# Kernel tuning notes

Hardware: AMD Instinct MI355X
Metric: run time of the kernel (lower is better)

The kernel has to match this reference:

```python
import jax, jax.numpy as jnp
import numpy as np

N, E, IN, H1, H2 = 100000, 3200000, 128, 64, 64


def setup_inputs() -> dict:
    key = jax.random.key(0)
    ks = jax.random.split(key, 6)
    return {
        "edge_index": jax.random.randint(ks[0], (2, E), 0, N),
        "edge_weight": jax.random.uniform(ks[1], (E,), jnp.float32),
        "emb": jax.random.normal(ks[2], (N, IN), jnp.float32) * 0.05,  # xavier-initialized node embeddings
        "W1": jax.random.normal(ks[3], (IN, H1), jnp.float32) / np.sqrt(IN),
        "b1": jnp.zeros((H1,), jnp.float32),
        "W2": jax.random.normal(ks[4], (H1, H2), jnp.float32) / np.sqrt(H1),
        "b2": jnp.zeros((H2,), jnp.float32),
    }


def _digcn_conv(x, edge_index, edge_weight, W, b):
    # DIGCNConv: dense transform, then weighted sparse neighborhood sum-aggregation.
    x = x @ W                                              # [N, d_out]
    msg = edge_weight[:, None] * x[edge_index[0]]          # gather sources -> [E, d_out]
    out = jax.ops.segment_sum(msg, edge_index[1], num_segments=x.shape[0])  # scatter-add to targets
    return out + b


def reference(edge_index, edge_weight, emb, W1, b1, W2, b2):
    h = jax.nn.relu(_digcn_conv(emb, edge_index, edge_weight, W1, b1))
    # F.dropout with training=False is identity (inference mode)
    return _digcn_conv(h, edge_index, edge_weight, W2, b2)
```

## Files before the change

### kernel.cpp

```cpp
#include <hip/hip_runtime.h>
#include <hip/hip_bf16.h>

#define NNODES 100000
#define DIN 128
#define DH 64
#define SRCMASK 0x1FFFF
#define BSH2 8
#define BN2 256
#define NBUCK2 ((NNODES + BN2 - 1) >> BSH2)
#define NCAP 8960
#define EPB 8192
#define MAXBLK 512
#define OVFCAP 4096

typedef short s16x8 __attribute__((ext_vector_type(8)));
typedef float f32x4 __attribute__((ext_vector_type(4)));

static __device__ __forceinline__ short f2bf(float f) {
  __hip_bfloat16 h = __float2bfloat16(f);
  return *reinterpret_cast<short*>(&h);
}
static __device__ __forceinline__ float bf2f(short s) {
  return __uint_as_float(((unsigned)(unsigned short)s) << 16);
}


__global__ __launch_bounds__(256, 4) void gemm1_mfma(
    const float* __restrict__ emb, const float* __restrict__ W1,
    __hip_bfloat16* __restrict__ x1, int N) {
  __shared__ short Bhi[4 * 4 * 64 * 8];
  __shared__ short Blo[4 * 4 * 64 * 8];
  int tid = threadIdx.x;

  for (int idx = tid; idx < 8192; idx += 256) {
    int i = idx & 7, ln = (idx >> 3) & 63, ct = (idx >> 9) & 3, kc = idx >> 11;
    int k = kc * 32 + (ln >> 4) * 8 + i;
    int col = ct * 16 + (ln & 15);
    float w = W1[k * DH + col];
    short h = f2bf(w);
    Bhi[idx] = h;
    Blo[idx] = f2bf(w - bf2f(h));
  }
  __syncthreads();

  int lane = tid & 63, wv = tid >> 6;
  int r0 = (blockIdx.x * 8 + wv * 2) * 16;
  if (r0 >= N) return;

  const int rA = lane & 15, g = lane >> 4;
  f32x4 acc[2][4] = {};

#pragma unroll
  for (int kc = 0; kc < 4; ++kc) {
    s16x8 ahi[2], alo[2];
#pragma unroll
    for (int rt = 0; rt < 2; ++rt) {
      int r = r0 + rt * 16 + rA;
      float av[8];
      if (r < N) {
        const float4* ap = (const float4*)(emb + (long)r * DIN + kc * 32 + g * 8);
        float4 v0 = ap[0], v1 = ap[1];
        av[0] = v0.x; av[1] = v0.y; av[2] = v0.z; av[3] = v0.w;
        av[4] = v1.x; av[5] = v1.y; av[6] = v1.z; av[7] = v1.w;
      } else {
#pragma unroll
        for (int i = 0; i < 8; ++i) av[i] = 0.f;
      }
#pragma unroll
      for (int i = 0; i < 8; ++i) {
        short h = f2bf(av[i]);
        ahi[rt][i] = h;
        alo[rt][i] = f2bf(av[i] - bf2f(h));
      }
    }
#pragma unroll
    for (int ct = 0; ct < 4; ++ct) {
      int fo = ((kc * 4 + ct) * 64 + lane) * 8;
      s16x8 bh = *(const s16x8*)&Bhi[fo];
      s16x8 bl = *(const s16x8*)&Blo[fo];
#pragma unroll
      for (int rt = 0; rt < 2; ++rt) {
        acc[rt][ct] = __builtin_amdgcn_mfma_f32_16x16x32_bf16(ahi[rt], bh, acc[rt][ct], 0, 0, 0);
        acc[rt][ct] = __builtin_amdgcn_mfma_f32_16x16x32_bf16(alo[rt], bh, acc[rt][ct], 0, 0, 0);
        acc[rt][ct] = __builtin_amdgcn_mfma_f32_16x16x32_bf16(ahi[rt], bl, acc[rt][ct], 0, 0, 0);
      }
    }
  }

#pragma unroll
  for (int rt = 0; rt < 2; ++rt) {
#pragma unroll
    for (int j = 0; j < 4; ++j) {
      int row = r0 + rt * 16 + g * 4 + j;
      if (row < N) {
#pragma unroll
        for (int ct = 0; ct < 4; ++ct)
          x1[(long)row * DH + ct * 16 + rA] = __float2bfloat16(acc[rt][ct][j]);
      }
    }
  }
}

__global__ __launch_bounds__(256, 4) void gemm2_mfma(
    const float* __restrict__ agg, const float* __restrict__ W2,
    const float* __restrict__ b1, __hip_bfloat16* __restrict__ x2, int N) {
  __shared__ short Bhi[2 * 4 * 64 * 8];
  __shared__ short Blo[2 * 4 * 64 * 8];
  int tid = threadIdx.x;

  for (int idx = tid; idx < 4096; idx += 256) {
    int i = idx & 7, ln = (idx >> 3) & 63, ct = (idx >> 9) & 3, kc = (idx >> 11) & 1;
    int k = kc * 32 + (ln >> 4) * 8 + i;
    int col = ct * 16 + (ln & 15);
    float w = W2[k * DH + col];
    short h = f2bf(w);
    Bhi[idx] = h;
    Blo[idx] = f2bf(w - bf2f(h));
  }
  __syncthreads();

  int lane = tid & 63, wv = tid >> 6;
  int r0 = (blockIdx.x * 8 + wv * 2) * 16;
  if (r0 >= N) return;

  const int rA = lane & 15, g = lane >> 4;
  f32x4 acc[2][4] = {};

#pragma unroll
  for (int kc = 0; kc < 2; ++kc) {
    const float4* bp = (const float4*)(b1 + kc * 32 + g * 8);
    float4 b0 = bp[0], b4 = bp[1];
    float bv[8] = {b0.x, b0.y, b0.z, b0.w, b4.x, b4.y, b4.z, b4.w};
    s16x8 ahi[2], alo[2];
#pragma unroll
    for (int rt = 0; rt < 2; ++rt) {
      int r = r0 + rt * 16 + rA;
      float av[8];
      if (r < N) {
        const float4* ap = (const float4*)(agg + (long)r * DH + kc * 32 + g * 8);
        float4 v0 = ap[0], v1 = ap[1];
        av[0] = v0.x; av[1] = v0.y; av[2] = v0.z; av[3] = v0.w;
        av[4] = v1.x; av[5] = v1.y; av[6] = v1.z; av[7] = v1.w;
      } else {
#pragma unroll
        for (int i = 0; i < 8; ++i) av[i] = -1e30f;
      }
#pragma unroll
      for (int i = 0; i < 8; ++i) {
        float a = fmaxf(av[i] + bv[i], 0.f);
        short h = f2bf(a);
        ahi[rt][i] = h;
        alo[rt][i] = f2bf(a - bf2f(h));
      }
    }
#pragma unroll
    for (int ct = 0; ct < 4; ++ct) {
      int fo = ((kc * 4 + ct) * 64 + lane) * 8;
      s16x8 bh = *(const s16x8*)&Bhi[fo];
      s16x8 bl = *(const s16x8*)&Blo[fo];
#pragma unroll
      for (int rt = 0; rt < 2; ++rt) {
        acc[rt][ct] = __builtin_amdgcn_mfma_f32_16x16x32_bf16(ahi[rt], bh, acc[rt][ct], 0, 0, 0);
        acc[rt][ct] = __builtin_amdgcn_mfma_f32_16x16x32_bf16(alo[rt], bh, acc[rt][ct], 0, 0, 0);
        acc[rt][ct] = __builtin_amdgcn_mfma_f32_16x16x32_bf16(ahi[rt], bl, acc[rt][ct], 0, 0, 0);
      }
    }
  }

#pragma unroll
  for (int rt = 0; rt < 2; ++rt) {
#pragma unroll
    for (int j = 0; j < 4; ++j) {
      int row = r0 + rt * 16 + g * 4 + j;
      if (row < N) {
#pragma unroll
        for (int ct = 0; ct < 4; ++ct)
          x2[(long)row * DH + ct * 16 + rA] = __float2bfloat16(acc[rt][ct][j]);
      }
    }
  }
}


__global__ __launch_bounds__(512, 6) void block_sort(
    const int* __restrict__ srcs, const int* __restrict__ dsts,
    const float* __restrict__ w, int* __restrict__ spk,
    unsigned char* __restrict__ sdl, unsigned short* __restrict__ offTab, int E) {
  __shared__ int stageP[EPB];
  __shared__ unsigned char stageD[EPB];
  __shared__ int hist[512];
  __shared__ int sc[512];
  __shared__ int cur[512];
  int tid = threadIdx.x, blk = blockIdx.x;
  int e0 = blk * EPB;

  hist[tid] = 0;
  __syncthreads();

  int pk[16], bd[16];
#pragma unroll
  for (int i = 0; i < 16; ++i) {
    int e = e0 + i * 512 + tid;
    if (e < E) {
      int s = srcs[e], d = dsts[e];
      float wv = w[e];
      int q = (int)(wv * 32768.f + 0.5f);
      if (q > 32767) q = 32767;
      pk[i] = (s & SRCMASK) | (q << 17);
      bd[i] = d;
    } else bd[i] = -1;
  }
#pragma unroll
  for (int i = 0; i < 16; ++i)
    if (bd[i] >= 0) atomicAdd(&hist[bd[i] >> BSH2], 1);
  __syncthreads();

  sc[tid] = (tid < NBUCK2) ? hist[tid] : 0;
  __syncthreads();
  for (int d = 1; d < 512; d <<= 1) {
    int u = (tid >= d) ? sc[tid - d] : 0;
    __syncthreads();
    sc[tid] += u;
    __syncthreads();
  }
  long row = (long)blk * (NBUCK2 + 1);
  if (tid < NBUCK2) {
    int base = sc[tid] - hist[tid];
    cur[tid] = base;
    offTab[row + tid] = (unsigned short)base;
    if (tid == NBUCK2 - 1) offTab[row + NBUCK2] = (unsigned short)sc[tid];
  }
  __syncthreads();

#pragma unroll
  for (int i = 0; i < 16; ++i) {
    if (bd[i] >= 0) {
      int pos = atomicAdd(&cur[bd[i] >> BSH2], 1);
      stageP[pos] = pk[i];
      stageD[pos] = (unsigned char)(bd[i] & (BN2 - 1));
    }
  }
  __syncthreads();

  int eN = min(EPB, E - e0);
  for (int i = tid; i < eN; i += 512) {
    spk[(long)blk * EPB + i] = stageP[i];
    sdl[(long)blk * EPB + i] = stageD[i];
  }
}

__global__ __launch_bounds__(512, 6) void sort_gemm1(
    const int* __restrict__ srcs, const int* __restrict__ dsts,
    const float* __restrict__ w, int* __restrict__ spk,
    unsigned char* __restrict__ sdl, unsigned short* __restrict__ offTab, int E,
    const float* __restrict__ emb, const float* __restrict__ W1,
    __hip_bfloat16* __restrict__ x1, int N, int NBLK, int* __restrict__ ovfcnt) {
  __shared__ __align__(16) char smem[EPB * 4 + EPB + 3 * 512 * 4];
  int tid = threadIdx.x;

  if (blockIdx.x >= (unsigned)NBLK) {
    if (blockIdx.x == (unsigned)NBLK && tid == 0) *ovfcnt = 0;
    short* Bhi = (short*)smem;
    short* Blo = Bhi + 8192;
    for (int idx = tid; idx < 8192; idx += 512) {
      int i = idx & 7, ln = (idx >> 3) & 63, ct = (idx >> 9) & 3, kc = idx >> 11;
      int k = kc * 32 + (ln >> 4) * 8 + i;
      int col = ct * 16 + (ln & 15);
      float wv = W1[k * DH + col];
      short h = f2bf(wv);
      Bhi[idx] = h;
      Blo[idx] = f2bf(wv - bf2f(h));
    }
    __syncthreads();

    int lane = tid & 63, wv8 = tid >> 6;
    int gblk = blockIdx.x - NBLK;
    int r0 = gblk * 256 + wv8 * 32;
    if (r0 >= N) return;

    const int rA = lane & 15, g = lane >> 4;
    f32x4 acc[2][4] = {};

#pragma unroll
    for (int kc = 0; kc < 4; ++kc) {
      s16x8 ahi[2], alo[2];
#pragma unroll
      for (int rt = 0; rt < 2; ++rt) {
        int r = r0 + rt * 16 + rA;
        float av[8];
        if (r < N) {
          const float4* ap = (const float4*)(emb + (long)r * DIN + kc * 32 + g * 8);
          float4 v0 = ap[0], v1 = ap[1];
          av[0] = v0.x; av[1] = v0.y; av[2] = v0.z; av[3] = v0.w;
          av[4] = v1.x; av[5] = v1.y; av[6] = v1.z; av[7] = v1.w;
        } else {
#pragma unroll
          for (int i = 0; i < 8; ++i) av[i] = 0.f;
        }
#pragma unroll
        for (int i = 0; i < 8; ++i) {
          short h = f2bf(av[i]);
          ahi[rt][i] = h;
          alo[rt][i] = f2bf(av[i] - bf2f(h));
        }
      }
#pragma unroll
      for (int ct = 0; ct < 4; ++ct) {
        int fo = ((kc * 4 + ct) * 64 + lane) * 8;
        s16x8 bh = *(const s16x8*)&Bhi[fo];
        s16x8 bl = *(const s16x8*)&Blo[fo];
#pragma unroll
        for (int rt = 0; rt < 2; ++rt) {
          acc[rt][ct] = __builtin_amdgcn_mfma_f32_16x16x32_bf16(ahi[rt], bh, acc[rt][ct], 0, 0, 0);
          acc[rt][ct] = __builtin_amdgcn_mfma_f32_16x16x32_bf16(alo[rt], bh, acc[rt][ct], 0, 0, 0);
          acc[rt][ct] = __builtin_amdgcn_mfma_f32_16x16x32_bf16(ahi[rt], bl, acc[rt][ct], 0, 0, 0);
        }
      }
    }

#pragma unroll
    for (int rt = 0; rt < 2; ++rt) {
#pragma unroll
      for (int j = 0; j < 4; ++j) {
        int row = r0 + rt * 16 + g * 4 + j;
        if (row < N) {
#pragma unroll
          for (int ct = 0; ct < 4; ++ct)
            x1[(long)row * DH + ct * 16 + rA] = __float2bfloat16(acc[rt][ct][j]);
        }
      }
    }
    return;
  }

  int* stageP = (int*)smem;
  unsigned char* stageD = (unsigned char*)(smem + EPB * 4);
  int* hist = (int*)(smem + EPB * 4 + EPB);
  int* sc   = hist + 512;
  int* cur  = sc + 512;
  int blk = blockIdx.x;
  int e0 = blk * EPB;

  hist[tid] = 0;
  __syncthreads();

  int pk[16], bd[16];
#pragma unroll
  for (int i = 0; i < 16; ++i) {
    int e = e0 + i * 512 + tid;
    if (e < E) {
      int s = srcs[e], d = dsts[e];
      float wv = w[e];
      int q = (int)(wv * 32768.f + 0.5f);
      if (q > 32767) q = 32767;
      pk[i] = (s & SRCMASK) | (q << 17);
      bd[i] = d;
    } else bd[i] = -1;
  }
#pragma unroll
  for (int i = 0; i < 16; ++i)
    if (bd[i] >= 0) atomicAdd(&hist[bd[i] >> BSH2], 1);
  __syncthreads();

  sc[tid] = (tid < NBUCK2) ? hist[tid] : 0;
  __syncthreads();
  for (int d = 1; d < 512; d <<= 1) {
    int u = (tid >= d) ? sc[tid - d] : 0;
    __syncthreads();
    sc[tid] += u;
    __syncthreads();
  }
  long row = (long)blk * (NBUCK2 + 1);
  if (tid < NBUCK2) {
    int base = sc[tid] - hist[tid];
    cur[tid] = base;
    offTab[row + tid] = (unsigned short)base;
    if (tid == NBUCK2 - 1) offTab[row + NBUCK2] = (unsigned short)sc[tid];
  }
  __syncthreads();

#pragma unroll
  for (int i = 0; i < 16; ++i) {
    if (bd[i] >= 0) {
      int pos = atomicAdd(&cur[bd[i] >> BSH2], 1);
      stageP[pos] = pk[i];
      stageD[pos] = (unsigned char)(bd[i] & (BN2 - 1));
    }
  }
  __syncthreads();

  int eN = min(EPB, E - e0);
  for (int i = tid; i < eN; i += 512) {
    spk[(long)blk * EPB + i] = stageP[i];
    sdl[(long)blk * EPB + i] = stageD[i];
  }
}

__global__ __launch_bounds__(512, 6) void gather_build(
    const unsigned short* __restrict__ offTab, const int* __restrict__ spk,
    const unsigned char* __restrict__ sdl,
    int* __restrict__ noff, int* __restrict__ ndeg, int* __restrict__ pairs,
    int2* __restrict__ ovf, int* __restrict__ ovfcnt, int NBLK, int N) {
  __shared__ int gathP[NCAP];
  __shared__ unsigned char gathD[NCAP];
  __shared__ unsigned short offR[MAXBLK];
  __shared__ unsigned short cntR[MAXBLK];
  __shared__ int baseR[MAXBLK];
  __shared__ int sc[512];
  __shared__ int deg[BN2], cur[BN2];
  int b = blockIdx.x, tid = threadIdx.x;

  for (int blk = tid; blk < NBLK; blk += 512) {
    long row = (long)blk * (NBUCK2 + 1);
    int st = offTab[row + b];
    int en = offTab[row + b + 1];
    offR[blk] = (unsigned short)st;
    cntR[blk] = (unsigned short)(en - st);
  }
  __syncthreads();

  sc[tid] = (tid < NBLK) ? (int)cntR[tid] : 0;
  __syncthreads();
  for (int d = 1; d < 512; d <<= 1) {
    int u = (tid >= d) ? sc[tid - d] : 0;
    __syncthreads();
    sc[tid] += u;
    __syncthreads();
  }
  if (tid < NBLK) baseR[tid] = sc[tid] - (int)cntR[tid];
  __syncthreads();
  int total = sc[NBLK - 1];
  int tcl = total > NCAP ? NCAP : total;

  for (int g = tid; g < total; g += 512) {
    int lo = 0, hi = NBLK - 1;
    while (lo < hi) {
      int mid = (lo + hi + 1) >> 1;
      if (baseR[mid] <= g) lo = mid; else hi = mid - 1;
    }
    int pos = (int)offR[lo] + (g - baseR[lo]);
    int pk = spk[(long)lo * EPB + pos];
    int dl = sdl[(long)lo * EPB + pos];
    if (g < NCAP) {
      gathP[g] = pk;
      gathD[g] = (unsigned char)dl;
    } else {
      int oi = atomicAdd(ovfcnt, 1);
      if (oi < OVFCAP) ovf[oi] = make_int2(pk, (b << BSH2) | dl);
    }
  }
  if (tid < BN2) deg[tid] = 0;
  __syncthreads();

  for (int k = tid; k < tcl; k += 512)
    atomicAdd(&deg[gathD[k]], 1);
  __syncthreads();

  sc[tid] = (tid < BN2) ? deg[tid] : 0;
  __syncthreads();
  for (int d = 1; d < 512; d <<= 1) {
    int u = (tid >= d) ? sc[tid - d] : 0;
    __syncthreads();
    sc[tid] += u;
    __syncthreads();
  }
  if (tid < BN2) {
    int excl = sc[tid] - deg[tid];
    int gpos = b * NCAP + excl;
    cur[tid] = gpos;
    int n = (b << BSH2) + tid;
    if (n < N) { noff[n] = gpos; ndeg[n] = deg[tid]; }
  }
  __syncthreads();

  for (int k = tid; k < tcl; k += 512) {
    int p = atomicAdd(&cur[gathD[k]], 1);
    pairs[p] = gathP[k];
  }
}

__global__ __launch_bounds__(256) void ovf_fixup(
    const int2* __restrict__ ovf, const int* __restrict__ ovfcnt,
    const short* __restrict__ x, float* __restrict__ out) {
  int cnt = *ovfcnt;
  if (cnt > OVFCAP) cnt = OVFCAP;
  int wid = (int)((blockIdx.x * 256 + threadIdx.x) >> 6);
  int lane = threadIdx.x & 63;
  int nw = (gridDim.x * 256) >> 6;
  for (int i = wid; i < cnt; i += nw) {
    int2 e = ovf[i];
    unsigned p = (unsigned)e.x;
    float wv = (float)(p >> 17) * (1.f / 32768.f);
    float xv = bf2f(x[(long)(p & SRCMASK) * DH + lane]);
    atomicAdd(&out[(long)e.y * DH + lane], wv * xv);
  }
}

#define ACC4(P, XV)                                          \
  do {                                                       \
    float wv_ = (float)((P) >> 17) * (1.f / 32768.f);        \
    a0 += wv_ * __uint_as_float((XV).x << 16);               \
    a1 += wv_ * __uint_as_float((XV).x & 0xFFFF0000u);       \
    a2 += wv_ * __uint_as_float((XV).y << 16);               \
    a3 += wv_ * __uint_as_float((XV).y & 0xFFFF0000u);       \
  } while (0)

__global__ __launch_bounds__(256) void agg_quad(
    const int* __restrict__ pairs, const int* __restrict__ noff,
    const int* __restrict__ ndeg,
    const uint2* __restrict__ x,
    const float* __restrict__ bias, float* __restrict__ out, int N) {
  int wid = (int)(((long)blockIdx.x * 256 + threadIdx.x) >> 6);
  int lane = threadIdx.x & 63;
  if (wid >= N) return;
  int h = lane >> 4;
  int fj = lane & 15;
  int st = noff[wid];
  int m = ndeg[wid];
  float a0 = 0.f, a1 = 0.f, a2 = 0.f, a3 = 0.f;

  for (int base = 0; base < m; base += 64) {
    int pl = (base + lane < m) ? pairs[st + base + lane] : 0;
    int mm = m - base;

    unsigned pg[8];
#pragma unroll
    for (int g = 0; g < 8; ++g) pg[g] = (unsigned)__shfl(pl, g * 4 + h);
    uint2 xg[8];
#pragma unroll
    for (int g = 0; g < 8; ++g) xg[g] = x[(pg[g] & SRCMASK) * 16 + fj];
#pragma unroll
    for (int g = 0; g < 8; ++g) ACC4(pg[g], xg[g]);

#pragma unroll
    for (int q = 32; q < 64; q += 16) {
      if (q >= mm) break;
      unsigned p0 = (unsigned)__shfl(pl, q + h);
      unsigned p1 = (unsigned)__shfl(pl, q + 4 + h);
      unsigned p2 = (unsigned)__shfl(pl, q + 8 + h);
      unsigned p3 = (unsigned)__shfl(pl, q + 12 + h);
      uint2 y0 = x[(p0 & SRCMASK) * 16 + fj];
      uint2 y1 = x[(p1 & SRCMASK) * 16 + fj];
      uint2 y2 = x[(p2 & SRCMASK) * 16 + fj];
      uint2 y3 = x[(p3 & SRCMASK) * 16 + fj];
      ACC4(p0, y0); ACC4(p1, y1); ACC4(p2, y2); ACC4(p3, y3);
    }
  }

  a0 += __shfl_xor(a0, 16); a0 += __shfl_xor(a0, 32);
  a1 += __shfl_xor(a1, 16); a1 += __shfl_xor(a1, 32);
  a2 += __shfl_xor(a2, 16); a2 += __shfl_xor(a2, 32);
  a3 += __shfl_xor(a3, 16); a3 += __shfl_xor(a3, 32);
  if (lane < 16) {
    if (bias) {
      float4 bv = ((const float4*)bias)[fj];
      a0 += bv.x; a1 += bv.y; a2 += bv.z; a3 += bv.w;
    }
    ((float4*)out)[(long)wid * 16 + fj] = make_float4(a0, a1, a2, a3);
  }
}


__global__ __launch_bounds__(256) void gemm1_f32(
    const float* __restrict__ emb, const float* __restrict__ W1,
    float* __restrict__ x1, int N) {
  __shared__ float Ws[DIN * DH];
  __shared__ float rows[4][DIN];
  int tid = threadIdx.x;
  for (int i = tid; i < DIN * DH; i += 256) Ws[i] = W1[i];
  int r0 = blockIdx.x * 4;
  for (int i = tid; i < 4 * DIN; i += 256) {
    int rr = i >> 7, kk = i & 127;
    int r = r0 + rr;
    rows[rr][kk] = (r < N) ? emb[(long)r * DIN + kk] : 0.f;
  }
  __syncthreads();
  int rr = tid >> 6, j = tid & 63;
  int r = r0 + rr;
  float acc = 0.f;
#pragma unroll
  for (int k = 0; k < DIN; ++k) acc += rows[rr][k] * Ws[k * DH + j];
  if (r < N) x1[(long)r * DH + j] = acc;
}

__global__ __launch_bounds__(256) void gemm2_f32(
    const float* __restrict__ agg, const float* __restrict__ W2,
    const float* __restrict__ b1, float* __restrict__ x2, int N) {
  __shared__ float Ws[DH * DH];
  __shared__ float rows[4][DH];
  int tid = threadIdx.x;
  for (int i = tid; i < DH * DH; i += 256) Ws[i] = W2[i];
  int r0 = blockIdx.x * 4;
  {
    int rr = tid >> 6, kk = tid & 63;
    int r = r0 + rr;
    float v = (r < N) ? agg[(long)r * DH + kk] + b1[kk] : 0.f;
    rows[rr][kk] = v > 0.f ? v : 0.f;
  }
  __syncthreads();
  int rr = tid >> 6, j = tid & 63;
  float acc = 0.f;
#pragma unroll
  for (int k = 0; k < DH; ++k) acc += rows[rr][k] * Ws[k * DH + j];
  int r = r0 + rr;
  if (r < N) x2[(long)r * DH + j] = acc;
}

__global__ __launch_bounds__(256) void init_bias_kernel(
    float* __restrict__ out, const float* __restrict__ b2, int total) {
  int i = blockIdx.x * 256 + threadIdx.x;
  if (i < total) out[i] = b2[i & 63];
}

__global__ __launch_bounds__(256) void scatter_kernel(
    const int* __restrict__ srcs, const int* __restrict__ dsts,
    const float* __restrict__ w, const float* __restrict__ x,
    float* __restrict__ out, int E) {
  long t = (long)blockIdx.x * 256 + threadIdx.x;
  long e = t >> 6;
  if (e >= E) return;
  int j = (int)(t & 63);
  int s = srcs[e];
  int d = dsts[e];
  float val = w[e] * x[(long)s * DH + j];
  atomicAdd(&out[(long)d * DH + j], val);
}


static inline size_t align256(size_t x) { return (x + 255) & ~(size_t)255; }

extern "C" void kernel_launch(void* const* d_in, const int* in_sizes, int n_in,
                              void* d_out, int out_size, void* d_ws, size_t ws_size,
                              hipStream_t stream) {
  const int*   edge_index = (const int*)d_in[0];
  const float* edge_w     = (const float*)d_in[1];
  const float* emb        = (const float*)d_in[2];
  const float* W1         = (const float*)d_in[3];
  const float* b1         = (const float*)d_in[4];
  const float* W2         = (const float*)d_in[5];
  const float* b2         = (const float*)d_in[6];
  float* out = (float*)d_out;

  const int E = in_sizes[0] / 2;
  const int N = NNODES;
  const int* srcs = edge_index;
  const int* dsts = edge_index + E;

  const int NBLK = (E + EPB - 1) / EPB;

  const size_t spkbytes    = (size_t)NBLK * EPB * sizeof(int);
  const size_t sdlbytes    = (size_t)NBLK * EPB;
  const size_t xbytes_bf   = (size_t)N * DH * sizeof(__hip_bfloat16);
  const size_t offTabbytes = (size_t)NBLK * (NBUCK2 + 1) * sizeof(unsigned short);
  const size_t pairsbytes  = (size_t)NBUCK2 * NCAP * sizeof(int);
  const size_t nbytes      = (size_t)N * sizeof(int);

  const int aggBlocks = (N + 3) / 4;
  const int gemmBlocks = (N + 127) / 128;
  const int g1Blocks   = (N + 255) / 256;

  size_t off = 0;
  char* base = (char*)d_ws;
  int* spk = (int*)(base + off);                   off = align256(off + spkbytes);
  unsigned char* sdl = (unsigned char*)(base + off); off = align256(off + sdlbytes);
  __hip_bfloat16* xbuf = (__hip_bfloat16*)(base + off); off = align256(off + xbytes_bf);
  unsigned short* offTab = (unsigned short*)(base + off); off = align256(off + offTabbytes);
  int* pairs = (int*)(base + off);  off = align256(off + pairsbytes);
  int* noff  = (int*)(base + off);  off = align256(off + nbytes);
  int* ndeg  = (int*)(base + off);  off = align256(off + nbytes);
  int2* ovf  = (int2*)(base + off); off = align256(off + OVFCAP * sizeof(int2));
  int* ovfcnt = (int*)(base + off); off = align256(off + 256);
  const size_t needed_fused = off;

  if (ws_size >= needed_fused && NBLK <= MAXBLK) {
    sort_gemm1<<<NBLK + g1Blocks, 512, 0, stream>>>(
        srcs, dsts, edge_w, spk, sdl, offTab, E, emb, W1, xbuf, N, NBLK, ovfcnt);
    gather_build<<<NBUCK2, 512, 0, stream>>>(offTab, spk, sdl, noff, ndeg, pairs,
                                             ovf, ovfcnt, NBLK, N);
    agg_quad<<<aggBlocks, 256, 0, stream>>>(pairs, noff, ndeg, (const uint2*)xbuf,
                                            nullptr, out, N);
    ovf_fixup<<<8, 256, 0, stream>>>(ovf, ovfcnt, (const short*)xbuf, out);
    gemm2_mfma<<<gemmBlocks, 256, 0, stream>>>(out, W2, b1, xbuf, N);
    agg_quad<<<aggBlocks, 256, 0, stream>>>(pairs, noff, ndeg, (const uint2*)xbuf,
                                            b2, out, N);
    ovf_fixup<<<8, 256, 0, stream>>>(ovf, ovfcnt, (const short*)xbuf, out);
    return;
  }

  off = 0;
  int* spk2 = (int*)(base + off);
  off = align256(off + (spkbytes > xbytes_bf ? spkbytes : xbytes_bf));
  __hip_bfloat16* xbuf2 = (__hip_bfloat16*)spk2;
  unsigned char* sdl2 = (unsigned char*)(base + off); off = align256(off + sdlbytes);
  unsigned short* offTab2 = (unsigned short*)(base + off); off = align256(off + offTabbytes);
  int* pairs2 = (int*)(base + off);  off = align256(off + pairsbytes);
  int* noff2  = (int*)(base + off);  off = align256(off + nbytes);
  int* ndeg2  = (int*)(base + off);  off = align256(off + nbytes);
  int2* ovf2  = (int2*)(base + off); off = align256(off + OVFCAP * sizeof(int2));
  int* ovfcnt2 = (int*)(base + off); off = align256(off + 256);
  const size_t needed_seq = off;

  if (ws_size >= needed_seq && NBLK <= MAXBLK) {
    hipMemsetAsync(ovfcnt2, 0, sizeof(int), stream);
    block_sort<<<NBLK, 512, 0, stream>>>(srcs, dsts, edge_w, spk2, sdl2, offTab2, E);
    gather_build<<<NBUCK2, 512, 0, stream>>>(offTab2, spk2, sdl2, noff2, ndeg2, pairs2,
                                             ovf2, ovfcnt2, NBLK, N);
    gemm1_mfma<<<gemmBlocks, 256, 0, stream>>>(emb, W1, xbuf2, N);
    agg_quad<<<aggBlocks, 256, 0, stream>>>(pairs2, noff2, ndeg2, (const uint2*)xbuf2,
                                            nullptr, out, N);
    ovf_fixup<<<8, 256, 0, stream>>>(ovf2, ovfcnt2, (const short*)xbuf2, out);
    gemm2_mfma<<<gemmBlocks, 256, 0, stream>>>(out, W2, b1, xbuf2, N);
    agg_quad<<<aggBlocks, 256, 0, stream>>>(pairs2, noff2, ndeg2, (const uint2*)xbuf2,
                                            b2, out, N);
    ovf_fixup<<<8, 256, 0, stream>>>(ovf2, ovfcnt2, (const short*)xbuf2, out);
    return;
  }

  const long scatterThreads = (long)E * 64;
  const int scatterBlocks = (int)((scatterThreads + 255) / 256);
  const int rowBlocks4 = (N + 3) / 4;
  float* xb1 = (float*)d_ws;

  gemm1_f32<<<rowBlocks4, 256, 0, stream>>>(emb, W1, xb1, N);
  hipMemsetAsync(d_out, 0, (size_t)N * DH * sizeof(float), stream);
  scatter_kernel<<<scatterBlocks, 256, 0, stream>>>(srcs, dsts, edge_w, xb1, out, E);

  gemm2_f32<<<rowBlocks4, 256, 0, stream>>>(out, W2, b1, xb1, N);
  init_bias_kernel<<<(N * DH + 255) / 256, 256, 0, stream>>>(out, b2, N * DH);
  scatter_kernel<<<scatterBlocks, 256, 0, stream>>>(srcs, dsts, edge_w, xb1, out, E);
}
```

Measured before the change: 182.0 us.

## Compact CSR pairs via global bucket totals, fuse GEMM1 into gather stage

Block sort now atomically accumulates per-bucket edge totals. The gather kernel prefix-sums these totals to place each bucket's pairs contiguously in a compact E-sized array instead of fixed NCAP-strided slots. Buckets that exceed the shared-memory capacity fall back to a two-pass direct global path, which removes the overflow list and both ovf_fixup launches. GEMM1 now runs alongside the gather stage instead of the sort stage, and an extra memset plus separate sort launch are added. Each gather block redundantly scans the bucket totals, and the fallback path rereads the sorted arrays twice.

```diff
diff --git a/kernel.cpp b/kernel.cpp
--- a/kernel.cpp
+++ b/kernel.cpp
@@ -8,10 +8,9 @@
 #define BSH2 8
 #define BN2 256
 #define NBUCK2 ((NNODES + BN2 - 1) >> BSH2)
-#define NCAP 8960
+#define NCAP 8448
 #define EPB 8192
 #define MAXBLK 512
-#define OVFCAP 4096
 
 typedef short s16x8 __attribute__((ext_vector_type(8)));
 typedef float f32x4 __attribute__((ext_vector_type(4)));
@@ -185,7 +184,8 @@
 __global__ __launch_bounds__(512, 6) void block_sort(
     const int* __restrict__ srcs, const int* __restrict__ dsts,
     const float* __restrict__ w, int* __restrict__ spk,
-    unsigned char* __restrict__ sdl, unsigned short* __restrict__ offTab, int E) {
+    unsigned char* __restrict__ sdl, unsigned short* __restrict__ offTab,
+    int* __restrict__ bTot, int E) {
   __shared__ int stageP[EPB];
   __shared__ unsigned char stageD[EPB];
   __shared__ int hist[512];
@@ -215,6 +215,8 @@
     if (bd[i] >= 0) atomicAdd(&hist[bd[i] >> BSH2], 1);
   __syncthreads();
 
+  if (tid < NBUCK2 && hist[tid]) atomicAdd(&bTot[tid], hist[tid]);
+
   sc[tid] = (tid < NBUCK2) ? hist[tid] : 0;
   __syncthreads();
   for (int d = 1; d < 512; d <<= 1) {
@@ -249,17 +251,18 @@
   }
 }
 
-__global__ __launch_bounds__(512, 6) void sort_gemm1(
-    const int* __restrict__ srcs, const int* __restrict__ dsts,
-    const float* __restrict__ w, int* __restrict__ spk,
-    unsigned char* __restrict__ sdl, unsigned short* __restrict__ offTab, int E,
+__global__ __launch_bounds__(512, 6) void gather_gemm1(
+    const unsigned short* __restrict__ offTab, const int* __restrict__ spk,
+    const unsigned char* __restrict__ sdl, const int* __restrict__ bTot,
+    int* __restrict__ noff, int* __restrict__ ndeg, int* __restrict__ pairs,
+    int NBLK, int N,
     const float* __restrict__ emb, const float* __restrict__ W1,
-    __hip_bfloat16* __restrict__ x1, int N, int NBLK, int* __restrict__ ovfcnt) {
-  __shared__ __align__(16) char smem[EPB * 4 + EPB + 3 * 512 * 4];
+    __hip_bfloat16* __restrict__ x1, int NB2) {
+  __shared__ __align__(16) char smem[50432];
+  __shared__ int shb;
   int tid = threadIdx.x;
 
-  if (blockIdx.x >= (unsigned)NBLK) {
-    if (blockIdx.x == (unsigned)NBLK && tid == 0) *ovfcnt = 0;
+  if ((int)blockIdx.x >= NB2) {
     short* Bhi = (short*)smem;
     short* Blo = Bhi + 8192;
     for (int idx = tid; idx < 8192; idx += 512) {
@@ -274,7 +277,7 @@
     __syncthreads();
 
     int lane = tid & 63, wv8 = tid >> 6;
-    int gblk = blockIdx.x - NBLK;
+    int gblk = blockIdx.x - NB2;
     int r0 = gblk * 256 + wv8 * 32;
     if (r0 >= N) return;
 
@@ -333,36 +336,17 @@
     return;
   }
 
-  int* stageP = (int*)smem;
-  unsigned char* stageD = (unsigned char*)(smem + EPB * 4);
-  int* hist = (int*)(smem + EPB * 4 + EPB);
-  int* sc   = hist + 512;
-  int* cur  = sc + 512;
-  int blk = blockIdx.x;
-  int e0 = blk * EPB;
-
-  hist[tid] = 0;
-  __syncthreads();
-
-  int pk[16], bd[16];
-#pragma unroll
-  for (int i = 0; i < 16; ++i) {
-    int e = e0 + i * 512 + tid;
-    if (e < E) {
-      int s = srcs[e], d = dsts[e];
-      float wv = w[e];
-      int q = (int)(wv * 32768.f + 0.5f);
-      if (q > 32767) q = 32767;
-      pk[i] = (s & SRCMASK) | (q << 17);
-      bd[i] = d;
-    } else bd[i] = -1;
-  }
-#pragma unroll
-  for (int i = 0; i < 16; ++i)
-    if (bd[i] >= 0) atomicAdd(&hist[bd[i] >> BSH2], 1);
-  __syncthreads();
-
-  sc[tid] = (tid < NBUCK2) ? hist[tid] : 0;
+  int b = blockIdx.x;
+  int* gathP = (int*)smem;
+  unsigned char* gathD = (unsigned char*)(smem + NCAP * 4);
+  unsigned short* offR = (unsigned short*)(smem + NCAP * 5);
+  unsigned short* cntR = offR + MAXBLK;
+  int* baseR = (int*)(smem + NCAP * 5 + MAXBLK * 4);
+  int* sc = baseR + MAXBLK;
+  int* deg = sc + 512;
+  int* cur = deg + BN2;
+
+  sc[tid] = (tid < NBUCK2) ? bTot[tid] : 0;
   __syncthreads();
   for (int d = 1; d < 512; d <<= 1) {
     int u = (tid >= d) ? sc[tid - d] : 0;
@@ -370,45 +354,9 @@
     sc[tid] += u;
     __syncthreads();
   }
-  long row = (long)blk * (NBUCK2 + 1);
-  if (tid < NBUCK2) {
-    int base = sc[tid] - hist[tid];
-    cur[tid] = base;
-    offTab[row + tid] = (unsigned short)base;
-    if (tid == NBUCK2 - 1) offTab[row + NBUCK2] = (unsigned short)sc[tid];
-  }
-  __syncthreads();
-
-#pragma unroll
-  for (int i = 0; i < 16; ++i) {
-    if (bd[i] >= 0) {
-      int pos = atomicAdd(&cur[bd[i] >> BSH2], 1);
-      stageP[pos] = pk[i];
-      stageD[pos] = (unsigned char)(bd[i] & (BN2 - 1));
-    }
-  }
-  __syncthreads();
-
-  int eN = min(EPB, E - e0);
-  for (int i = tid; i < eN; i += 512) {
-    spk[(long)blk * EPB + i] = stageP[i];
-    sdl[(long)blk * EPB + i] = stageD[i];
-  }
-}
-
-__global__ __launch_bounds__(512, 6) void gather_build(
-    const unsigned short* __restrict__ offTab, const int* __restrict__ spk,
-    const unsigned char* __restrict__ sdl,
-    int* __restrict__ noff, int* __restrict__ ndeg, int* __restrict__ pairs,
-    int2* __restrict__ ovf, int* __restrict__ ovfcnt, int NBLK, int N) {
-  __shared__ int gathP[NCAP];
-  __shared__ unsigned char gathD[NCAP];
-  __shared__ unsigned short offR[MAXBLK];
-  __shared__ unsigned short cntR[MAXBLK];
-  __shared__ int baseR[MAXBLK];
-  __shared__ int sc[512];
-  __shared__ int deg[BN2], cur[BN2];
-  int b = blockIdx.x, tid = threadIdx.x;
+  if (tid == 0) shb = (b == 0) ? 0 : sc[b - 1];
+  __syncthreads();
+  int bstart = shb;
 
   for (int blk = tid; blk < NBLK; blk += 512) {
     long row = (long)blk * (NBUCK2 + 1);
@@ -418,7 +366,6 @@
     cntR[blk] = (unsigned short)(en - st);
   }
   __syncthreads();
-
   sc[tid] = (tid < NBLK) ? (int)cntR[tid] : 0;
   __syncthreads();
   for (int d = 1; d < 512; d <<= 1) {
@@ -428,71 +375,82 @@
     __syncthreads();
   }
   if (tid < NBLK) baseR[tid] = sc[tid] - (int)cntR[tid];
+  if (tid < BN2) deg[tid] = 0;
   __syncthreads();
   int total = sc[NBLK - 1];
-  int tcl = total > NCAP ? NCAP : total;
-
-  for (int g = tid; g < total; g += 512) {
-    int lo = 0, hi = NBLK - 1;
-    while (lo < hi) {
-      int mid = (lo + hi + 1) >> 1;
-      if (baseR[mid] <= g) lo = mid; else hi = mid - 1;
-    }
-    int pos = (int)offR[lo] + (g - baseR[lo]);
-    int pk = spk[(long)lo * EPB + pos];
-    int dl = sdl[(long)lo * EPB + pos];
-    if (g < NCAP) {
-      gathP[g] = pk;
-      gathD[g] = (unsigned char)dl;
-    } else {
-      int oi = atomicAdd(ovfcnt, 1);
-      if (oi < OVFCAP) ovf[oi] = make_int2(pk, (b << BSH2) | dl);
-    }
-  }
-  if (tid < BN2) deg[tid] = 0;
-  __syncthreads();
-
-  for (int k = tid; k < tcl; k += 512)
-    atomicAdd(&deg[gathD[k]], 1);
-  __syncthreads();
-
-  sc[tid] = (tid < BN2) ? deg[tid] : 0;
-  __syncthreads();
-  for (int d = 1; d < 512; d <<= 1) {
-    int u = (tid >= d) ? sc[tid - d] : 0;
-    __syncthreads();
-    sc[tid] += u;
-    __syncthreads();
-  }
-  if (tid < BN2) {
-    int excl = sc[tid] - deg[tid];
-    int gpos = b * NCAP + excl;
-    cur[tid] = gpos;
-    int n = (b << BSH2) + tid;
-    if (n < N) { noff[n] = gpos; ndeg[n] = deg[tid]; }
-  }
-  __syncthreads();
-
-  for (int k = tid; k < tcl; k += 512) {
-    int p = atomicAdd(&cur[gathD[k]], 1);
-    pairs[p] = gathP[k];
-  }
-}
-
-__global__ __launch_bounds__(256) void ovf_fixup(
-    const int2* __restrict__ ovf, const int* __restrict__ ovfcnt,
-    const short* __restrict__ x, float* __restrict__ out) {
-  int cnt = *ovfcnt;
-  if (cnt > OVFCAP) cnt = OVFCAP;
-  int wid = (int)((blockIdx.x * 256 + threadIdx.x) >> 6);
-  int lane = threadIdx.x & 63;
-  int nw = (gridDim.x * 256) >> 6;
-  for (int i = wid; i < cnt; i += nw) {
-    int2 e = ovf[i];
-    unsigned p = (unsigned)e.x;
-    float wv = (float)(p >> 17) * (1.f / 32768.f);
-    float xv = bf2f(x[(long)(p & SRCMASK) * DH + lane]);
-    atomicAdd(&out[(long)e.y * DH + lane], wv * xv);
+
+  if (total <= NCAP) {
+    for (int g = tid; g < total; g += 512) {
+      int lo = 0, hi = NBLK - 1;
+      while (lo < hi) {
+        int mid = (lo + hi + 1) >> 1;
+        if (baseR[mid] <= g) lo = mid; else hi = mid - 1;
+      }
+      int pos = (int)offR[lo] + (g - baseR[lo]);
+      gathP[g] = spk[(long)lo * EPB + pos];
+      gathD[g] = sdl[(long)lo * EPB + pos];
+    }
+    __syncthreads();
+    for (int k = tid; k < total; k += 512)
+      atomicAdd(&deg[gathD[k]], 1);
+    __syncthreads();
+    sc[tid] = (tid < BN2) ? deg[tid] : 0;
+    __syncthreads();
+    for (int d = 1; d < 512; d <<= 1) {
+      int u = (tid >= d) ? sc[tid - d] : 0;
+      __syncthreads();
+      sc[tid] += u;
+      __syncthreads();
+    }
+    if (tid < BN2) {
+      int excl = sc[tid] - deg[tid];
+      cur[tid] = bstart + excl;
+      int n = (b << BSH2) + tid;
+      if (n < N) { noff[n] = bstart + excl; ndeg[n] = deg[tid]; }
+    }
+    __syncthreads();
+    for (int k = tid; k < total; k += 512) {
+      int p = atomicAdd(&cur[gathD[k]], 1);
+      pairs[p] = gathP[k];
+    }
+  } else {
+    for (int g = tid; g < total; g += 512) {
+      int lo = 0, hi = NBLK - 1;
+      while (lo < hi) {
+        int mid = (lo + hi + 1) >> 1;
+        if (baseR[mid] <= g) lo = mid; else hi = mid - 1;
+      }
+      int pos = (int)offR[lo] + (g - baseR[lo]);
+      atomicAdd(&deg[sdl[(long)lo * EPB + pos]], 1);
+    }
+    __syncthreads();
+    sc[tid] = (tid < BN2) ? deg[tid] : 0;
+    __syncthreads();
+    for (int d = 1; d < 512; d <<= 1) {
+      int u = (tid >= d) ? sc[tid - d] : 0;
+      __syncthreads();
+      sc[tid] += u;
+      __syncthreads();
+    }
+    if (tid < BN2) {
+      int excl = sc[tid] - deg[tid];
+      cur[tid] = bstart + excl;
+      int n = (b << BSH2) + tid;
+      if (n < N) { noff[n] = bstart + excl; ndeg[n] = deg[tid]; }
+    }
+    __syncthreads();
+    for (int g = tid; g < total; g += 512) {
+      int lo = 0, hi = NBLK - 1;
+      while (lo < hi) {
+        int mid = (lo + hi + 1) >> 1;
+        if (baseR[mid] <= g) lo = mid; else hi = mid - 1;
+      }
+      int pos = (int)offR[lo] + (g - baseR[lo]);
+      int pk = spk[(long)lo * EPB + pos];
+      int dl = sdl[(long)lo * EPB + pos];
+      int p = atomicAdd(&cur[dl], 1);
+      pairs[p] = pk;
+    }
   }
 }
 
@@ -652,7 +610,7 @@
   const size_t sdlbytes    = (size_t)NBLK * EPB;
   const size_t xbytes_bf   = (size_t)N * DH * sizeof(__hip_bfloat16);
   const size_t offTabbytes = (size_t)NBLK * (NBUCK2 + 1) * sizeof(unsigned short);
-  const size_t pairsbytes  = (size_t)NBUCK2 * NCAP * sizeof(int);
+  const size_t pairsbytes  = (size_t)E * sizeof(int);
   const size_t nbytes      = (size_t)N * sizeof(int);
 
   const int aggBlocks = (N + 3) / 4;
@@ -668,22 +626,19 @@
   int* pairs = (int*)(base + off);  off = align256(off + pairsbytes);
   int* noff  = (int*)(base + off);  off = align256(off + nbytes);
   int* ndeg  = (int*)(base + off);  off = align256(off + nbytes);
-  int2* ovf  = (int2*)(base + off); off = align256(off + OVFCAP * sizeof(int2));
-  int* ovfcnt = (int*)(base + off); off = align256(off + 256);
+  int* bTot  = (int*)(base + off);  off = align256(off + NBUCK2 * sizeof(int));
   const size_t needed_fused = off;
 
   if (ws_size >= needed_fused && NBLK <= MAXBLK) {
-    sort_gemm1<<<NBLK + g1Blocks, 512, 0, stream>>>(
-        srcs, dsts, edge_w, spk, sdl, offTab, E, emb, W1, xbuf, N, NBLK, ovfcnt);
-    gather_build<<<NBUCK2, 512, 0, stream>>>(offTab, spk, sdl, noff, ndeg, pairs,
-                                             ovf, ovfcnt, NBLK, N);
+    hipMemsetAsync(bTot, 0, NBUCK2 * sizeof(int), stream);
+    block_sort<<<NBLK, 512, 0, stream>>>(srcs, dsts, edge_w, spk, sdl, offTab, bTot, E);
+    gather_gemm1<<<NBUCK2 + g1Blocks, 512, 0, stream>>>(
+        offTab, spk, sdl, bTot, noff, ndeg, pairs, NBLK, N, emb, W1, xbuf, NBUCK2);
     agg_quad<<<aggBlocks, 256, 0, stream>>>(pairs, noff, ndeg, (const uint2*)xbuf,
                                             nullptr, out, N);
-    ovf_fixup<<<8, 256, 0, stream>>>(ovf, ovfcnt, (const short*)xbuf, out);
     gemm2_mfma<<<gemmBlocks, 256, 0, stream>>>(out, W2, b1, xbuf, N);
     agg_quad<<<aggBlocks, 256, 0, stream>>>(pairs, noff, ndeg, (const uint2*)xbuf,
                                             b2, out, N);
-    ovf_fixup<<<8, 256, 0, stream>>>(ovf, ovfcnt, (const short*)xbuf, out);
     return;
   }
 
@@ -696,23 +651,20 @@
   int* pairs2 = (int*)(base + off);  off = align256(off + pairsbytes);
   int* noff2  = (int*)(base + off);  off = align256(off + nbytes);
   int* ndeg2  = (int*)(base + off);  off = align256(off + nbytes);
-  int2* ovf2  = (int2*)(base + off); off = align256(off + OVFCAP * sizeof(int2));
-  int* ovfcnt2 = (int*)(base + off); off = align256(off + 256);
+  int* bTot2  = (int*)(base + off);  off = align256(off + NBUCK2 * sizeof(int));
   const size_t needed_seq = off;
 
   if (ws_size >= needed_seq && NBLK <= MAXBLK) {
-    hipMemsetAsync(ovfcnt2, 0, sizeof(int), stream);
-    block_sort<<<NBLK, 512, 0, stream>>>(srcs, dsts, edge_w, spk2, sdl2, offTab2, E);
-    gather_build<<<NBUCK2, 512, 0, stream>>>(offTab2, spk2, sdl2, noff2, ndeg2, pairs2,
-                                             ovf2, ovfcnt2, NBLK, N);
+    hipMemsetAsync(bTot2, 0, NBUCK2 * sizeof(int), stream);
+    block_sort<<<NBLK, 512, 0, stream>>>(srcs, dsts, edge_w, spk2, sdl2, offTab2, bTot2, E);
+    gather_gemm1<<<NBUCK2, 512, 0, stream>>>(
+        offTab2, spk2, sdl2, bTot2, noff2, ndeg2, pairs2, NBLK, N, emb, W1, xbuf2, NBUCK2);
     gemm1_mfma<<<gemmBlocks, 256, 0, stream>>>(emb, W1, xbuf2, N);
     agg_quad<<<aggBlocks, 256, 0, stream>>>(pairs2, noff2, ndeg2, (const uint2*)xbuf2,
                                             nullptr, out, N);
-    ovf_fixup<<<8, 256, 0, stream>>>(ovf2, ovfcnt2, (const short*)xbuf2, out);
     gemm2_mfma<<<gemmBlocks, 256, 0, stream>>>(out, W2, b1, xbuf2, N);
     agg_quad<<<aggBlocks, 256, 0, stream>>>(pairs2, noff2, ndeg2, (const uint2*)xbuf2,
                                             b2, out, N);
-    ovf_fixup<<<8, 256, 0, stream>>>(ovf2, ovfcnt2, (const short*)xbuf2, out);
     return;
   }
 
```

New measurement: 186.6 us. +2.5%, slower.
